# Performance work log

Measured on AMD Instinct MI355X. Metric: run time of the kernel, lower is better.

The kernel has to match this reference:

```python
import jax, jax.numpy as jnp
import numpy as np

B, S, D, H, DFF = 2, 2048, 1024, 16, 4096
DK = D // H
EPS = 1e-05


def setup_inputs() -> dict:
    key = jax.random.key(0)
    ks = jax.random.split(key, 10)
    s = 0.02
    return {
        "x": jax.random.normal(ks[0], (B, S, D), jnp.float32),
        "src_mask": jnp.ones((B, 1, 1, S), jnp.int32),
        "wq": jax.random.normal(ks[1], (D, D), jnp.float32) * s,
        "wk": jax.random.normal(ks[2], (D, D), jnp.float32) * s,
        "wv": jax.random.normal(ks[3], (D, D), jnp.float32) * s,
        "wo": jax.random.normal(ks[4], (D, D), jnp.float32) * s,
        "w1": jax.random.normal(ks[5], (D, DFF), jnp.float32) * s,
        "b1": jnp.zeros((DFF,), jnp.float32),
        "w2": jax.random.normal(ks[6], (DFF, D), jnp.float32) * s,
        "b2": jnp.zeros((D,), jnp.float32),
        "gamma1": jnp.ones((), jnp.float32),
        "beta1": jnp.ones((), jnp.float32),
        "gamma2": jnp.ones((), jnp.float32),
        "beta2": jnp.ones((), jnp.float32),
    }


def layer_norm(x, gamma, beta):
    # torch.var uses unbiased estimator (ddof=1); gamma/beta are scalars
    mean = jnp.mean(x, axis=-1, keepdims=True)
    var = jnp.var(x, axis=-1, keepdims=True, ddof=1)
    return (x - mean) * gamma / jnp.sqrt(var + EPS) + beta


def mha(x, wq, wk, wv, wo):
    # Note: source's masked_fill is non-in-place with discarded result -> mask has no effect.
    q = (x @ wq).reshape(B, S, H, DK).transpose(0, 2, 1, 3)
    k = (x @ wk).reshape(B, S, H, DK).transpose(0, 2, 1, 3)
    v = (x @ wv).reshape(B, S, H, DK).transpose(0, 2, 1, 3)
    scores = jnp.einsum('bhqd,bhkd->bhqk', q, k) / jnp.sqrt(jnp.float32(DK))
    attn = jax.nn.softmax(scores, axis=-1)
    out = jnp.einsum('bhqk,bhkd->bhqd', attn, v)
    out = out.transpose(0, 2, 1, 3).reshape(B, S, D)
    return out @ wo


def reference(x, src_mask, wq, wk, wv, wo, w1, b1, w2, b2,
              gamma1, beta1, gamma2, beta2):
    # residual 1: attention (dropout = identity in eval)
    x = layer_norm(x + mha(x, wq, wk, wv, wo), gamma1, beta1)
    # residual 2: FFN
    ff = jax.nn.relu(x @ w1 + b1) @ w2 + b2
    x = layer_norm(x + ff, gamma2, beta2)
    return x
```

## Files before the change

kernel.cpp:

```cpp
#include <hip/hip_runtime.h>
#include <cstdio>

constexpr int B_   = 2;
constexpr int S_   = 2048;
constexpr int D_   = 1024;
constexpr int H_   = 16;
constexpr int DFF_ = 4096;
constexpr int DK_  = D_ / H_;
constexpr int M_   = B_ * S_;
constexpr float EPS_ = 1e-5f;
constexpr size_t MEGE = 1u << 20;
constexpr size_t QKV_STRIDE = 4 * MEGE;

typedef __attribute__((ext_vector_type(8))) short bf16x8;
typedef __attribute__((ext_vector_type(4))) float f32x4;

__device__ __forceinline__ float bf2f(unsigned int u) {
    return __uint_as_float(u << 16);
}
__device__ __forceinline__ unsigned short f2bf(float f) {
    unsigned int u = __float_as_uint(f);
    unsigned int r = u + 0x7fffu + ((u >> 16) & 1u);
    return (unsigned short)(r >> 16);
}
__device__ __forceinline__ unsigned short f2bf_rz(float f) {
    return (unsigned short)(__float_as_uint(f) >> 16);
}

__device__ __forceinline__ void gload_lds16(const unsigned short* g, unsigned short* l) {
    __builtin_amdgcn_global_load_lds(
        (const __attribute__((address_space(1))) unsigned int*)g,
        (__attribute__((address_space(3))) unsigned int*)l, 16, 0, 0);
}

__global__ __launch_bounds__(256)
void tconv_k(const float* __restrict__ W, unsigned short* __restrict__ Wt, int K, int N)
{
    __shared__ float t[32][33];
    const int tx = threadIdx.x & 31, ty = threadIdx.x >> 5;
    const int n0 = blockIdx.x * 32, k0 = blockIdx.y * 32;
    #pragma unroll
    for (int p = 0; p < 4; ++p)
        t[ty + p * 8][tx] = W[(size_t)(k0 + ty + p * 8) * N + n0 + tx];
    __syncthreads();
    #pragma unroll
    for (int p = 0; p < 4; ++p)
        Wt[(size_t)(n0 + ty + p * 8) * K + k0 + tx] = f2bf(t[tx][ty + p * 8]);
}

__global__ __launch_bounds__(256)
void tconv4_k(const float* __restrict__ a, const float* __restrict__ b,
              const float* __restrict__ c, const float* __restrict__ d,
              unsigned short* __restrict__ oa, unsigned short* __restrict__ ob,
              unsigned short* __restrict__ oc, unsigned short* __restrict__ od)
{
    const int z = blockIdx.z;
    const float* W = (z == 0) ? a : (z == 1) ? b : (z == 2) ? c : d;
    unsigned short* Wt = (z == 0) ? oa : (z == 1) ? ob : (z == 2) ? oc : od;
    __shared__ float t[32][33];
    const int tx = threadIdx.x & 31, ty = threadIdx.x >> 5;
    const int n0 = blockIdx.x * 32, k0 = blockIdx.y * 32;
    #pragma unroll
    for (int p = 0; p < 4; ++p)
        t[ty + p * 8][tx] = W[(size_t)(k0 + ty + p * 8) * D_ + n0 + tx];
    __syncthreads();
    #pragma unroll
    for (int p = 0; p < 4; ++p)
        Wt[(size_t)(n0 + ty + p * 8) * D_ + k0 + tx] = f2bf(t[tx][ty + p * 8]);
}

__global__ __launch_bounds__(256)
void cvtx_k(const float* __restrict__ in, unsigned short* __restrict__ out) {
    int i = blockIdx.x * 256 + threadIdx.x;
    float4 f = reinterpret_cast<const float4*>(in)[i];
    ushort4 u;
    u.x = f2bf(f.x); u.y = f2bf(f.y); u.z = f2bf(f.z); u.w = f2bf(f.w);
    reinterpret_cast<ushort4*>(out)[i] = u;
}

template<int BM, int OMODE, bool RELU>
__global__ __launch_bounds__(512, 2)
void mg2_k(const unsigned short* __restrict__ A,
           const unsigned short* __restrict__ Bt,
           const float* __restrict__ bias,
           unsigned short* __restrict__ C,
           int M, int N, int K, int Kld)
{
    constexpr int MI  = BM / 64;
    constexpr int AMH = (BM == 128) ? 2 : 1;
    __shared__ __align__(16) unsigned short As[2][BM * 64];
    __shared__ __align__(16) unsigned short Bs[2][256 * 64];

    const int z = blockIdx.z;
    A  += (size_t)z * K;
    Bt += (size_t)z * K;
    C  += (size_t)z * ((size_t)M * N);

    const int tid  = threadIdx.x;
    const int w    = tid >> 6, lane = tid & 63;
    const int l15  = lane & 15, quad = lane >> 4;
    const int wm   = w >> 2, wn = w & 3;
    const int m0   = blockIdx.y * BM, n0 = blockIdx.x * 256;
    const int NT   = K >> 6;

    const int srow = lane >> 3;
    const int schk = (lane & 7) ^ srow;
    const int rsw  = l15 & 7;

    f32x4 acc[2][MI][2][2];
    #pragma unroll
    for (int mh = 0; mh < 2; ++mh)
        #pragma unroll
        for (int mi = 0; mi < MI; ++mi)
            #pragma unroll
            for (int nh = 0; nh < 2; ++nh)
                #pragma unroll
                for (int nj = 0; nj < 2; ++nj)
                    acc[mh][mi][nh][nj] = (f32x4){0.f, 0.f, 0.f, 0.f};

    bf16x8 aA[AMH][MI][2];
    bf16x8 b0[2][2], b1[2][2];

    auto stage = [&](int tile, int type) {
        if (tile >= NT) return;
        const int buf = tile & 1;
        unsigned short* dst; const unsigned short* src; int r0;
        if (BM == 256) {
            if      (type == 0) { dst = &As[buf][0];        src = A;  r0 = m0; }
            else if (type == 1) { dst = &Bs[buf][0];        src = Bt; r0 = n0; }
            else if (type == 2) { dst = &Bs[buf][128 * 64]; src = Bt; r0 = n0 + 128; }
            else                { dst = &As[buf][128 * 64]; src = A;  r0 = m0 + 128; }
        } else {
            if      (type == 0) { dst = &Bs[buf][0];        src = Bt; r0 = n0; }
            else if (type == 1) { dst = &As[buf][0];        src = A;  r0 = m0; }
            else                { dst = &Bs[buf][128 * 64]; src = Bt; r0 = n0 + 128; }
        }
        const int k0 = tile * 64;
        #pragma unroll
        for (int g = 0; g < 2; ++g) {
            const int r = w * 16 + g * 8 + srow;
            gload_lds16(src + (size_t)(r0 + r) * Kld + k0 + schk * 8,
                        dst + (w * 16 + g * 8) * 64);
        }
    };
    auto rdA = [&](int buf, int mh, int amh) {
        const unsigned short* base = &As[buf][(BM == 256 && mh) ? 128 * 64 : 0];
        #pragma unroll
        for (int mi = 0; mi < MI; ++mi) {
            const int row = (BM == 256) ? (wm * 64 + mi * 16 + l15)
                                        : (wm * 64 + mh * 32 + mi * 16 + l15);
            const unsigned short* rp = base + row * 64;
            aA[amh][mi][0] = *reinterpret_cast<const bf16x8*>(rp + ((quad    ) ^ rsw) * 8);
            aA[amh][mi][1] = *reinterpret_cast<const bf16x8*>(rp + ((quad + 4) ^ rsw) * 8);
        }
    };
    auto rdB = [&](int buf, int nh, bf16x8 (&b)[2][2]) {
        const unsigned short* base = &Bs[buf][nh ? 128 * 64 : 0];
        #pragma unroll
        for (int nj = 0; nj < 2; ++nj) {
            const int row = wn * 32 + nj * 16 + l15;
            const unsigned short* rp = base + row * 64;
            b[nj][0] = *reinterpret_cast<const bf16x8*>(rp + ((quad    ) ^ rsw) * 8);
            b[nj][1] = *reinterpret_cast<const bf16x8*>(rp + ((quad + 4) ^ rsw) * 8);
        }
    };
    auto mm = [&](int mh, int amh, int nh, bf16x8 (&b)[2][2]) {
        __builtin_amdgcn_s_setprio(1);
        #pragma unroll
        for (int mi = 0; mi < MI; ++mi)
            #pragma unroll
            for (int nj = 0; nj < 2; ++nj) {
                acc[mh][mi][nh][nj] = __builtin_amdgcn_mfma_f32_16x16x32_bf16(
                    aA[amh][mi][0], b[nj][0], acc[mh][mi][nh][nj], 0, 0, 0);
                acc[mh][mi][nh][nj] = __builtin_amdgcn_mfma_f32_16x16x32_bf16(
                    aA[amh][mi][1], b[nj][1], acc[mh][mi][nh][nj], 0, 0, 0);
            }
        __builtin_amdgcn_s_setprio(0);
    };

    if (BM == 256) {
        stage(0, 0); stage(0, 1); stage(0, 2); stage(0, 3);
        stage(1, 0); stage(1, 1); stage(1, 2);
    } else {
        stage(0, 0); stage(0, 1); stage(0, 2);
        stage(1, 0); stage(1, 1);
    }

    for (int t = 0; t < NT; ++t) {
        const int cur = t & 1;
        if (t == NT - 1)    asm volatile("s_waitcnt vmcnt(0)" ::: "memory");
        else if (BM == 256) asm volatile("s_waitcnt vmcnt(6)" ::: "memory");
        else                asm volatile("s_waitcnt vmcnt(4)" ::: "memory");
        __builtin_amdgcn_s_barrier();

        if (BM == 256) {
            rdA(cur, 0, 0); rdB(cur, 0, b0); stage(t + 1, 3);
            __builtin_amdgcn_s_barrier();
            asm volatile("s_waitcnt lgkmcnt(0)" ::: "memory");
            mm(0, 0, 0, b0);
            __builtin_amdgcn_s_barrier();
            rdB(cur, 1, b1); stage(t + 2, 0);
            __builtin_amdgcn_s_barrier();
            asm volatile("s_waitcnt lgkmcnt(0)" ::: "memory");
            mm(0, 0, 1, b1);
            __builtin_amdgcn_s_barrier();
            rdA(cur, 1, 0); stage(t + 2, 1);
            __builtin_amdgcn_s_barrier();
            asm volatile("s_waitcnt lgkmcnt(0)" ::: "memory");
            mm(1, 0, 0, b0);
            __builtin_amdgcn_s_barrier();
            stage(t + 2, 2);
            __builtin_amdgcn_s_barrier();
            asm volatile("s_waitcnt lgkmcnt(0)" ::: "memory");
            mm(1, 0, 1, b1);
        } else {
            rdA(cur, 0, 0); rdA(cur, 1, 1); rdB(cur, 0, b0); stage(t + 1, 2);
            __builtin_amdgcn_s_barrier();
            asm volatile("s_waitcnt lgkmcnt(0)" ::: "memory");
            mm(0, 0, 0, b0); mm(1, 1, 0, b0);
            __builtin_amdgcn_s_barrier();
            rdB(cur, 1, b1); stage(t + 2, 0); stage(t + 2, 1);
            __builtin_amdgcn_s_barrier();
            asm volatile("s_waitcnt lgkmcnt(0)" ::: "memory");
            mm(0, 0, 1, b1); mm(1, 1, 1, b1);
        }
    }

    #pragma unroll
    for (int mh = 0; mh < 2; ++mh)
        #pragma unroll
        for (int mi = 0; mi < MI; ++mi) {
            const int mrow = (BM == 256) ? (mh * 128 + wm * 64 + mi * 16)
                                         : (wm * 64 + mh * 32 + mi * 16);
            #pragma unroll
            for (int r = 0; r < 4; ++r) {
                const int m = m0 + mrow + quad * 4 + r;
                #pragma unroll
                for (int nh = 0; nh < 2; ++nh)
                    #pragma unroll
                    for (int nj = 0; nj < 2; ++nj) {
                        const int n = n0 + nh * 128 + wn * 32 + nj * 16 + l15;
                        float v = acc[mh][mi][nh][nj][r];
                        if (bias) v += bias[n];
                        if (RELU) v = fmaxf(v, 0.0f);
                        size_t o;
                        if (OMODE == 2) {
                            int mat = n >> 10, nn = n & 1023;
                            int b = m >> 11, s = m & 2047;
                            int h = nn >> 6, dk = nn & 63;
                            o = (size_t)mat * QKV_STRIDE + (((size_t)b * H_ + h) * S_ + s) * DK_ + dk;
                        } else {
                            o = (size_t)m * N + n;
                        }
                        C[o] = f2bf(v);
                    }
            }
        }
}

__device__ __forceinline__ float wave_sum(float v) {
    #pragma unroll
    for (int off = 32; off > 0; off >>= 1) v += __shfl_down(v, off, 64);
    return v;
}

constexpr int TQ_ = 128;
constexpr int TK_ = 64;
constexpr int LP_ = 72;
constexpr int NT_ = S_ / TK_;

__global__ __launch_bounds__(256)
void fattn_k(const unsigned short* __restrict__ Qm, const unsigned short* __restrict__ Km,
             const unsigned short* __restrict__ Vm, unsigned short* __restrict__ O)
{
    const int bh  = blockIdx.x >> 4;
    const int qt  = blockIdx.x & 15;
    const int tid = threadIdx.x;
    const int w = tid >> 6, lane = tid & 63;
    const int quad = lane >> 4, l15 = lane & 15;

    __shared__ unsigned short Ks[2][TK_][LP_];
    __shared__ unsigned short Vt[2][DK_ + 16][LP_];
    __shared__ unsigned short Ps[4][32][LP_];

    bf16x8 qf[2][2];
    #pragma unroll
    for (int i = 0; i < 2; ++i) {
        const unsigned short* qp = Qm + ((size_t)bh * S_ + qt * TQ_ + w * 32 + i * 16 + l15) * DK_;
        qf[i][0] = *reinterpret_cast<const bf16x8*>(qp + quad * 8);
        qf[i][1] = *reinterpret_cast<const bf16x8*>(qp + 32 + quad * 8);
    }

    f32x4 o[2][4];
    f32x4 o4[2];
    #pragma unroll
    for (int i = 0; i < 2; ++i) {
        #pragma unroll
        for (int n = 0; n < 4; ++n) o[i][n] = (f32x4){0.f, 0.f, 0.f, 0.f};
        o4[i] = (f32x4){0.f, 0.f, 0.f, 0.f};
    }

    const unsigned short* kg0 = Km + (size_t)bh * S_ * DK_;
    const unsigned short* vg0 = Vm + (size_t)bh * S_ * DK_;
    const int dgrp = tid >> 4;
    const int vkp  = tid & 15;

    {
        const uint4* kg = reinterpret_cast<const uint4*>(kg0);
        #pragma unroll
        for (int p = 0; p < 2; ++p) {
            int idx = p * 256 + tid;
            *reinterpret_cast<uint4*>(&Ks[0][idx >> 3][(idx & 7) * 8]) = kg[idx];
        }
        ushort4 vp[4];
        #pragma unroll
        for (int p = 0; p < 4; ++p)
            vp[p] = reinterpret_cast<const ushort4*>(vg0 + (size_t)(vkp + p * 16) * DK_)[dgrp];
        ushort4 pk;
        pk.x = vp[0].x; pk.y = vp[1].x; pk.z = vp[2].x; pk.w = vp[3].x;
        *reinterpret_cast<ushort4*>(&Vt[0][dgrp * 4 + 0][vkp * 4]) = pk;
        pk.x = vp[0].y; pk.y = vp[1].y; pk.z = vp[2].y; pk.w = vp[3].y;
        *reinterpret_cast<ushort4*>(&Vt[0][dgrp * 4 + 1][vkp * 4]) = pk;
        pk.x = vp[0].z; pk.y = vp[1].z; pk.z = vp[2].z; pk.w = vp[3].z;
        *reinterpret_cast<ushort4*>(&Vt[0][dgrp * 4 + 2][vkp * 4]) = pk;
        pk.x = vp[0].w; pk.y = vp[1].w; pk.z = vp[2].w; pk.w = vp[3].w;
        *reinterpret_cast<ushort4*>(&Vt[0][dgrp * 4 + 3][vkp * 4]) = pk;
        for (int idx = tid; idx < 2 * 16 * LP_; idx += 256) {
            int b  = idx / (16 * LP_);
            int rr = (idx / LP_) % 16;
            int cc = idx % LP_;
            Vt[b][64 + rr][cc] = (rr == 0) ? (unsigned short)0x3F80 : (unsigned short)0;
        }
    }

    for (int t = 0; t < NT_; ++t) {
        const int cur = t & 1, nxt = cur ^ 1;
        __syncthreads();

        uint4 kpre0, kpre1;
        ushort4 vp[4];
        const bool hn = (t + 1 < NT_);
        if (hn) {
            const uint4* kg = reinterpret_cast<const uint4*>(kg0 + (size_t)(t + 1) * TK_ * DK_);
            kpre0 = kg[tid];
            kpre1 = kg[256 + tid];
            const unsigned short* vg = vg0 + (size_t)(t + 1) * TK_ * DK_;
            #pragma unroll
            for (int p = 0; p < 4; ++p)
                vp[p] = reinterpret_cast<const ushort4*>(vg + (size_t)(vkp + p * 16) * DK_)[dgrp];
        }

        f32x4 s[2][4];
        #pragma unroll
        for (int n = 0; n < 4; ++n) {
            bf16x8 b0 = *reinterpret_cast<const bf16x8*>(&Ks[cur][n * 16 + l15][quad * 8]);
            bf16x8 b1 = *reinterpret_cast<const bf16x8*>(&Ks[cur][n * 16 + l15][32 + quad * 8]);
            #pragma unroll
            for (int i = 0; i < 2; ++i) {
                f32x4 a2 = (f32x4){0.f, 0.f, 0.f, 0.f};
                a2 = __builtin_amdgcn_mfma_f32_16x16x32_bf16(qf[i][0], b0, a2, 0, 0, 0);
                a2 = __builtin_amdgcn_mfma_f32_16x16x32_bf16(qf[i][1], b1, a2, 0, 0, 0);
                s[i][n] = a2;
            }
        }

        #pragma unroll
        for (int i = 0; i < 2; ++i)
            #pragma unroll
            for (int r = 0; r < 4; ++r) {
                ushort4 pk;
                pk.x = f2bf_rz(__expf(s[i][0][r] * 0.125f));
                pk.y = f2bf_rz(__expf(s[i][1][r] * 0.125f));
                pk.z = f2bf_rz(__expf(s[i][2][r] * 0.125f));
                pk.w = f2bf_rz(__expf(s[i][3][r] * 0.125f));
                *reinterpret_cast<ushort4*>(&Ps[w][i * 16 + quad * 4 + r][l15 * 4]) = pk;
            }

        if (hn) {
            *reinterpret_cast<uint4*>(&Ks[nxt][tid >> 3][(tid & 7) * 8]) = kpre0;
            int idx = 256 + tid;
            *reinterpret_cast<uint4*>(&Ks[nxt][idx >> 3][(idx & 7) * 8]) = kpre1;
            ushort4 pk;
            pk.x = vp[0].x; pk.y = vp[1].x; pk.z = vp[2].x; pk.w = vp[3].x;
            *reinterpret_cast<ushort4*>(&Vt[nxt][dgrp * 4 + 0][vkp * 4]) = pk;
            pk.x = vp[0].y; pk.y = vp[1].y; pk.z = vp[2].y; pk.w = vp[3].y;
            *reinterpret_cast<ushort4*>(&Vt[nxt][dgrp * 4 + 1][vkp * 4]) = pk;
            pk.x = vp[0].z; pk.y = vp[1].z; pk.z = vp[2].z; pk.w = vp[3].z;
            *reinterpret_cast<ushort4*>(&Vt[nxt][dgrp * 4 + 2][vkp * 4]) = pk;
            pk.x = vp[0].w; pk.y = vp[1].w; pk.z = vp[2].w; pk.w = vp[3].w;
            *reinterpret_cast<ushort4*>(&Vt[nxt][dgrp * 4 + 3][vkp * 4]) = pk;
        }
        __syncthreads();

        bf16x8 pa[2][2];
        #pragma unroll
        for (int i = 0; i < 2; ++i) {
            pa[i][0] = *reinterpret_cast<const bf16x8*>(&Ps[w][i * 16 + l15][quad * 8]);
            pa[i][1] = *reinterpret_cast<const bf16x8*>(&Ps[w][i * 16 + l15][32 + quad * 8]);
        }
        #pragma unroll
        for (int n = 0; n < 4; ++n) {
            bf16x8 vb0 = *reinterpret_cast<const bf16x8*>(&Vt[cur][n * 16 + l15][quad * 8]);
            bf16x8 vb1 = *reinterpret_cast<const bf16x8*>(&Vt[cur][n * 16 + l15][32 + quad * 8]);
            #pragma unroll
            for (int i = 0; i < 2; ++i) {
                o[i][n] = __builtin_amdgcn_mfma_f32_16x16x32_bf16(pa[i][0], vb0, o[i][n], 0, 0, 0);
                o[i][n] = __builtin_amdgcn_mfma_f32_16x16x32_bf16(pa[i][1], vb1, o[i][n], 0, 0, 0);
            }
        }
        {
            bf16x8 vb40 = *reinterpret_cast<const bf16x8*>(&Vt[cur][64 + l15][quad * 8]);
            bf16x8 vb41 = *reinterpret_cast<const bf16x8*>(&Vt[cur][64 + l15][32 + quad * 8]);
            #pragma unroll
            for (int i = 0; i < 2; ++i) {
                o4[i] = __builtin_amdgcn_mfma_f32_16x16x32_bf16(pa[i][0], vb40, o4[i], 0, 0, 0);
                o4[i] = __builtin_amdgcn_mfma_f32_16x16x32_bf16(pa[i][1], vb41, o4[i], 0, 0, 0);
            }
        }
    }

    const int b = bh >> 4, h = bh & 15;
    #pragma unroll
    for (int i = 0; i < 2; ++i)
        #pragma unroll
        for (int r = 0; r < 4; ++r) {
            float lrv = __shfl(o4[i][r], lane & 0x30, 64);
            float inv = 1.0f / lrv;
            int q = qt * TQ_ + w * 32 + i * 16 + quad * 4 + r;
            unsigned short* op = O + ((size_t)b * S_ + q) * D_ + h * DK_;
            #pragma unroll
            for (int n = 0; n < 4; ++n)
                op[n * 16 + l15] = f2bf(o[i][n][r] * inv);
        }
}

template<bool HAS_BIAS, bool RES_F32, bool OUT_F32>
__global__ __launch_bounds__(256)
void lnr_k(const unsigned short* __restrict__ P0, const unsigned short* __restrict__ P1,
           const void* __restrict__ res, const float* __restrict__ bias,
           const float* __restrict__ gp, const float* __restrict__ bp,
           void* __restrict__ Out)
{
    const int row = blockIdx.x;
    const int tid = threadIdx.x;
    const int lane = tid & 63, wave = tid >> 6;
    __shared__ float rs[4], rss[4];

    const size_t i4 = (size_t)row * 256 + tid;
    const ushort4 a = reinterpret_cast<const ushort4*>(P0)[i4];
    const ushort4 b = reinterpret_cast<const ushort4*>(P1)[i4];
    float v0 = bf2f(a.x) + bf2f(b.x);
    float v1 = bf2f(a.y) + bf2f(b.y);
    float v2 = bf2f(a.z) + bf2f(b.z);
    float v3 = bf2f(a.w) + bf2f(b.w);
    if (RES_F32) {
        float4 rv = reinterpret_cast<const float4*>(res)[i4];
        v0 += rv.x; v1 += rv.y; v2 += rv.z; v3 += rv.w;
    } else {
        ushort4 rv = reinterpret_cast<const ushort4*>(res)[i4];
        v0 += bf2f(rv.x); v1 += bf2f(rv.y); v2 += bf2f(rv.z); v3 += bf2f(rv.w);
    }
    if (HAS_BIAS) {
        float4 bv = reinterpret_cast<const float4*>(bias)[tid];
        v0 += bv.x; v1 += bv.y; v2 += bv.z; v3 += bv.w;
    }

    float s  = v0 + v1 + v2 + v3;
    float ss = v0*v0 + v1*v1 + v2*v2 + v3*v3;
    s = wave_sum(s);
    ss = wave_sum(ss);
    if (lane == 0) { rs[wave] = s; rss[wave] = ss; }
    __syncthreads();
    const float stot  = rs[0] + rs[1] + rs[2] + rs[3];
    const float sstot = rss[0] + rss[1] + rss[2] + rss[3];
    const float mean = stot / (float)D_;
    const float var  = (sstot - (float)D_ * mean * mean) / (float)(D_ - 1);
    const float scl = gp[0] * rsqrtf(var + EPS_);
    const float be = bp[0];

    float o0 = (v0 - mean) * scl + be;
    float o1 = (v1 - mean) * scl + be;
    float o2 = (v2 - mean) * scl + be;
    float o3 = (v3 - mean) * scl + be;
    if (OUT_F32) {
        reinterpret_cast<float4*>(Out)[i4] = make_float4(o0, o1, o2, o3);
    } else {
        ushort4 o;
        o.x = f2bf(o0); o.y = f2bf(o1); o.z = f2bf(o2); o.w = f2bf(o3);
        reinterpret_cast<ushort4*>(Out)[i4] = o;
    }
}

extern "C" void kernel_launch(void* const* d_in, const int* in_sizes, int n_in,
                              void* d_out, int out_size, void* d_ws, size_t ws_size,
                              hipStream_t stream)
{
    const float* x   = (const float*)d_in[0];
    const float* wq  = (const float*)d_in[2];
    const float* wk  = (const float*)d_in[3];
    const float* wv  = (const float*)d_in[4];
    const float* wo  = (const float*)d_in[5];
    const float* w1  = (const float*)d_in[6];
    const float* b1  = (const float*)d_in[7];
    const float* w2  = (const float*)d_in[8];
    const float* b2  = (const float*)d_in[9];
    const float* g1  = (const float*)d_in[10];
    const float* be1 = (const float*)d_in[11];
    const float* g2  = (const float*)d_in[12];
    const float* be2 = (const float*)d_in[13];

    unsigned short* ws = (unsigned short*)d_ws;
    const size_t need_bytes = 32 * MEGE * 2;
    if (ws_size < need_bytes) {
        fprintf(stderr, "kernel_launch: ws too small (%zu < %zu)\n", ws_size, need_bytes);
    }
    unsigned short* wqt = ws + 0 * MEGE;
    unsigned short* wkt = ws + 1 * MEGE;
    unsigned short* wvt = ws + 2 * MEGE;
    unsigned short* wot = ws + 3 * MEGE;
    unsigned short* w1t = ws + 4 * MEGE;
    unsigned short* w2t = ws + 8 * MEGE;
    unsigned short* xb  = ws + 12 * MEGE;
    unsigned short* Q   = ws + 16 * MEGE;
    unsigned short* K   = ws + 20 * MEGE;
    unsigned short* V   = ws + 24 * MEGE;
    unsigned short* AO  = ws + 28 * MEGE;
    unsigned short* x1  = xb;
    unsigned short* WP  = ws + 16 * MEGE;
    unsigned short* h1  = ws + 16 * MEGE;
    unsigned short* FP  = ws + 0 * MEGE;

    tconv4_k<<<dim3(D_ / 32, D_ / 32, 4), 256, 0, stream>>>(wq, wk, wv, wo, wqt, wkt, wvt, wot);
    tconv_k<<<dim3(DFF_ / 32, D_ / 32), 256, 0, stream>>>(w1, w1t, D_, DFF_);
    tconv_k<<<dim3(D_ / 32, DFF_ / 32), 256, 0, stream>>>(w2, w2t, DFF_, D_);
    cvtx_k<<<dim3(M_ * D_ / 1024), 256, 0, stream>>>(x, xb);

    mg2_k<256, 2, false><<<dim3(3 * D_ / 256, M_ / 256), 512, 0, stream>>>(
        xb, wqt, nullptr, Q, M_, 3 * D_, D_, D_);

    fattn_k<<<dim3(B_ * H_ * (S_ / TQ_)), 256, 0, stream>>>(Q, K, V, AO);

    mg2_k<128, 0, false><<<dim3(D_ / 256, M_ / 128, 2), 512, 0, stream>>>(
        AO, wot, nullptr, WP, M_, D_, D_ / 2, D_);

    lnr_k<false, true, false><<<dim3(M_), 256, 0, stream>>>(
        WP, WP + 4 * MEGE, x, nullptr, g1, be1, x1);

    mg2_k<256, 0, true><<<dim3(DFF_ / 256, M_ / 256), 512, 0, stream>>>(
        x1, w1t, b1, h1, M_, DFF_, D_, D_);

    mg2_k<128, 0, false><<<dim3(D_ / 256, M_ / 128, 2), 512, 0, stream>>>(
        h1, w2t, nullptr, FP, M_, D_, DFF_ / 2, DFF_);

    lnr_k<true, false, true><<<dim3(M_), 256, 0, stream>>>(
        FP, FP + 4 * MEGE, x1, b2, g2, be2, d_out);
}
```

Measured before the change: 347.4 us.

## Swizzle attention LDS tiles, async K staging, drop a barrier, fuse prep kernels

Replaces the padded LDS tiles in the flash-attention kernel with XOR-swizzled 64-wide layouts. K tiles are now staged with direct global-to-LDS loads, and the mid-iteration barrier between P writes and P/V reads is removed. MFMA sections get raised wave priority. The four weight/input conversion kernels are merged into one launch. The intent is to cut LDS bank conflicts, register staging and launch overhead; the removed barrier risks ordering hazards, since Vt[nxt] and Ks[nxt] writes still rely on the top-of-loop barrier.

After: 342.3 us. Within noise of the previous version (-1.5%).

```diff
diff --git a/kernel.cpp b/kernel.cpp
--- a/kernel.cpp
+++ b/kernel.cpp
@@ -33,49 +33,50 @@
         (__attribute__((address_space(3))) unsigned int*)l, 16, 0, 0);
 }
 
+__device__ __forceinline__ void tr32(const float* __restrict__ W, unsigned short* __restrict__ Wt,
+                                     int K, int N, int bx, int by, float* t )
+{
+    const int tx = threadIdx.x & 31, ty = threadIdx.x >> 5;
+    const int n0 = bx * 32, k0 = by * 32;
+    #pragma unroll
+    for (int p = 0; p < 4; ++p)
+        t[(ty + p * 8) * 33 + tx] = W[(size_t)(k0 + ty + p * 8) * N + n0 + tx];
+    __syncthreads();
+    #pragma unroll
+    for (int p = 0; p < 4; ++p)
+        Wt[(size_t)(n0 + ty + p * 8) * K + k0 + tx] = f2bf(t[tx * 33 + ty + p * 8]);
+}
+
 __global__ __launch_bounds__(256)
-void tconv_k(const float* __restrict__ W, unsigned short* __restrict__ Wt, int K, int N)
+void prep_k(const float* __restrict__ wq, const float* __restrict__ wk,
+            const float* __restrict__ wv, const float* __restrict__ wo,
+            const float* __restrict__ w1, const float* __restrict__ w2,
+            const float* __restrict__ x,
+            unsigned short* __restrict__ wqt, unsigned short* __restrict__ wkt,
+            unsigned short* __restrict__ wvt, unsigned short* __restrict__ wot,
+            unsigned short* __restrict__ w1t, unsigned short* __restrict__ w2t,
+            unsigned short* __restrict__ xb)
 {
-    __shared__ float t[32][33];
-    const int tx = threadIdx.x & 31, ty = threadIdx.x >> 5;
-    const int n0 = blockIdx.x * 32, k0 = blockIdx.y * 32;
-    #pragma unroll
-    for (int p = 0; p < 4; ++p)
-        t[ty + p * 8][tx] = W[(size_t)(k0 + ty + p * 8) * N + n0 + tx];
-    __syncthreads();
-    #pragma unroll
-    for (int p = 0; p < 4; ++p)
-        Wt[(size_t)(n0 + ty + p * 8) * K + k0 + tx] = f2bf(t[tx][ty + p * 8]);
-}
-
-__global__ __launch_bounds__(256)
-void tconv4_k(const float* __restrict__ a, const float* __restrict__ b,
-              const float* __restrict__ c, const float* __restrict__ d,
-              unsigned short* __restrict__ oa, unsigned short* __restrict__ ob,
-              unsigned short* __restrict__ oc, unsigned short* __restrict__ od)
-{
-    const int z = blockIdx.z;
-    const float* W = (z == 0) ? a : (z == 1) ? b : (z == 2) ? c : d;
-    unsigned short* Wt = (z == 0) ? oa : (z == 1) ? ob : (z == 2) ? oc : od;
-    __shared__ float t[32][33];
-    const int tx = threadIdx.x & 31, ty = threadIdx.x >> 5;
-    const int n0 = blockIdx.x * 32, k0 = blockIdx.y * 32;
-    #pragma unroll
-    for (int p = 0; p < 4; ++p)
-        t[ty + p * 8][tx] = W[(size_t)(k0 + ty + p * 8) * D_ + n0 + tx];
-    __syncthreads();
-    #pragma unroll
-    for (int p = 0; p < 4; ++p)
-        Wt[(size_t)(n0 + ty + p * 8) * D_ + k0 + tx] = f2bf(t[tx][ty + p * 8]);
-}
-
-__global__ __launch_bounds__(256)
-void cvtx_k(const float* __restrict__ in, unsigned short* __restrict__ out) {
-    int i = blockIdx.x * 256 + threadIdx.x;
-    float4 f = reinterpret_cast<const float4*>(in)[i];
-    ushort4 u;
-    u.x = f2bf(f.x); u.y = f2bf(f.y); u.z = f2bf(f.z); u.w = f2bf(f.w);
-    reinterpret_cast<ushort4*>(out)[i] = u;
+    __shared__ float t[32 * 33];
+    const int bid = blockIdx.x;
+    if (bid < 4096) {
+        const int z = bid >> 10, rem = bid & 1023;
+        const float* W = (z == 0) ? wq : (z == 1) ? wk : (z == 2) ? wv : wo;
+        unsigned short* Wt = (z == 0) ? wqt : (z == 1) ? wkt : (z == 2) ? wvt : wot;
+        tr32(W, Wt, D_, D_, rem & 31, rem >> 5, t);
+    } else if (bid < 8192) {
+        const int rem = bid - 4096;
+        tr32(w1, w1t, D_, DFF_, rem & 127, rem >> 7, t);
+    } else if (bid < 12288) {
+        const int rem = bid - 8192;
+        tr32(w2, w2t, DFF_, D_, rem & 31, rem >> 5, t);
+    } else {
+        const int i = (bid - 12288) * 256 + threadIdx.x;
+        float4 f = reinterpret_cast<const float4*>(x)[i];
+        ushort4 u;
+        u.x = f2bf(f.x); u.y = f2bf(f.y); u.z = f2bf(f.z); u.w = f2bf(f.w);
+        reinterpret_cast<ushort4*>(xb)[i] = u;
+    }
 }
 
 template<int BM, int OMODE, bool RELU>
@@ -266,7 +267,6 @@
 
 constexpr int TQ_ = 128;
 constexpr int TK_ = 64;
-constexpr int LP_ = 72;
 constexpr int NT_ = S_ / TK_;
 
 __global__ __launch_bounds__(256)
@@ -278,10 +278,11 @@
     const int tid = threadIdx.x;
     const int w = tid >> 6, lane = tid & 63;
     const int quad = lane >> 4, l15 = lane & 15;
-
-    __shared__ unsigned short Ks[2][TK_][LP_];
-    __shared__ unsigned short Vt[2][DK_ + 16][LP_];
-    __shared__ unsigned short Ps[4][32][LP_];
+    const int sw = l15 & 7;
+
+    __shared__ __align__(16) unsigned short Ks[2][TK_][64];
+    __shared__ __align__(16) unsigned short Vt[2][80][64];
+    __shared__ __align__(16) unsigned short Ps[4][32][64];
 
     bf16x8 qf[2][2];
     #pragma unroll
@@ -304,32 +305,48 @@
     const unsigned short* vg0 = Vm + (size_t)bh * S_ * DK_;
     const int dgrp = tid >> 4;
     const int vkp  = tid & 15;
-
-    {
-        const uint4* kg = reinterpret_cast<const uint4*>(kg0);
-        #pragma unroll
-        for (int p = 0; p < 2; ++p) {
-            int idx = p * 256 + tid;
-            *reinterpret_cast<uint4*>(&Ks[0][idx >> 3][(idx & 7) * 8]) = kg[idx];
-        }
-        ushort4 vp[4];
+    const int srow = lane >> 3;
+    const int schk = (lane & 7) ^ srow;
+
+    auto stageK = [&](int t, int buf) {
+        const unsigned short* src = kg0 + (size_t)t * TK_ * DK_;
+        #pragma unroll
+        for (int g = 0; g < 2; ++g) {
+            const int r0 = w * 16 + g * 8;
+            gload_lds16(src + (size_t)(r0 + srow) * DK_ + schk * 8, &Ks[buf][r0][0]);
+        }
+    };
+    auto loadV = [&](int t, ushort4 (&vp)[4]) {
+        const unsigned short* vg = vg0 + (size_t)t * TK_ * DK_;
         #pragma unroll
         for (int p = 0; p < 4; ++p)
-            vp[p] = reinterpret_cast<const ushort4*>(vg0 + (size_t)(vkp + p * 16) * DK_)[dgrp];
+            vp[p] = reinterpret_cast<const ushort4*>(vg + (size_t)(vkp + p * 16) * DK_)[dgrp];
+    };
+    auto storeVt = [&](int buf, ushort4 (&vp)[4]) {
+        char* base = reinterpret_cast<char*>(&Vt[buf][dgrp * 4][0]);
+        const int cs = vkp >> 1, ch = (vkp & 1) << 3;
         ushort4 pk;
         pk.x = vp[0].x; pk.y = vp[1].x; pk.z = vp[2].x; pk.w = vp[3].x;
-        *reinterpret_cast<ushort4*>(&Vt[0][dgrp * 4 + 0][vkp * 4]) = pk;
+        *reinterpret_cast<ushort4*>(base + 0 * 128 + (((cs ^ ((dgrp * 4 + 0) & 7)) << 4) + ch)) = pk;
         pk.x = vp[0].y; pk.y = vp[1].y; pk.z = vp[2].y; pk.w = vp[3].y;
-        *reinterpret_cast<ushort4*>(&Vt[0][dgrp * 4 + 1][vkp * 4]) = pk;
+        *reinterpret_cast<ushort4*>(base + 1 * 128 + (((cs ^ ((dgrp * 4 + 1) & 7)) << 4) + ch)) = pk;
         pk.x = vp[0].z; pk.y = vp[1].z; pk.z = vp[2].z; pk.w = vp[3].z;
-        *reinterpret_cast<ushort4*>(&Vt[0][dgrp * 4 + 2][vkp * 4]) = pk;
+        *reinterpret_cast<ushort4*>(base + 2 * 128 + (((cs ^ ((dgrp * 4 + 2) & 7)) << 4) + ch)) = pk;
         pk.x = vp[0].w; pk.y = vp[1].w; pk.z = vp[2].w; pk.w = vp[3].w;
-        *reinterpret_cast<ushort4*>(&Vt[0][dgrp * 4 + 3][vkp * 4]) = pk;
-        for (int idx = tid; idx < 2 * 16 * LP_; idx += 256) {
-            int b  = idx / (16 * LP_);
-            int rr = (idx / LP_) % 16;
-            int cc = idx % LP_;
-            Vt[b][64 + rr][cc] = (rr == 0) ? (unsigned short)0x3F80 : (unsigned short)0;
+        *reinterpret_cast<ushort4*>(base + 3 * 128 + (((cs ^ ((dgrp * 4 + 3) & 7)) << 4) + ch)) = pk;
+    };
+
+    stageK(0, 0);
+    {
+        ushort4 vp0[4];
+        loadV(0, vp0);
+        storeVt(0, vp0);
+        for (int idx = tid; idx < 2 * 16 * 64; idx += 256) {
+            const int b  = idx >> 10;
+            const int rr = (idx >> 6) & 15;
+            const int cc = idx & 63;
+            Vt[b][64 + rr][((cc >> 3) ^ (rr & 7)) * 8 + (cc & 7)] =
+                (rr == 0) ? (unsigned short)0x3F80 : (unsigned short)0;
         }
     }
 
@@ -337,24 +354,17 @@
         const int cur = t & 1, nxt = cur ^ 1;
         __syncthreads();
 
-        uint4 kpre0, kpre1;
+        const bool hn = (t + 1 < NT_);
         ushort4 vp[4];
-        const bool hn = (t + 1 < NT_);
-        if (hn) {
-            const uint4* kg = reinterpret_cast<const uint4*>(kg0 + (size_t)(t + 1) * TK_ * DK_);
-            kpre0 = kg[tid];
-            kpre1 = kg[256 + tid];
-            const unsigned short* vg = vg0 + (size_t)(t + 1) * TK_ * DK_;
-            #pragma unroll
-            for (int p = 0; p < 4; ++p)
-                vp[p] = reinterpret_cast<const ushort4*>(vg + (size_t)(vkp + p * 16) * DK_)[dgrp];
-        }
+        if (hn) { stageK(t + 1, nxt); loadV(t + 1, vp); }
 
         f32x4 s[2][4];
+        __builtin_amdgcn_s_setprio(1);
         #pragma unroll
         for (int n = 0; n < 4; ++n) {
-            bf16x8 b0 = *reinterpret_cast<const bf16x8*>(&Ks[cur][n * 16 + l15][quad * 8]);
-            bf16x8 b1 = *reinterpret_cast<const bf16x8*>(&Ks[cur][n * 16 + l15][32 + quad * 8]);
+            const unsigned short* kp = &Ks[cur][n * 16 + l15][0];
+            bf16x8 b0 = *reinterpret_cast<const bf16x8*>(kp + ((quad ^ sw) << 3));
+            bf16x8 b1 = *reinterpret_cast<const bf16x8*>(kp + (((quad + 4) ^ sw) << 3));
             #pragma unroll
             for (int i = 0; i < 2; ++i) {
                 f32x4 a2 = (f32x4){0.f, 0.f, 0.f, 0.f};
@@ -363,6 +373,7 @@
                 s[i][n] = a2;
             }
         }
+        __builtin_amdgcn_s_setprio(0);
 
         #pragma unroll
         for (int i = 0; i < 2; ++i)
@@ -373,35 +384,27 @@
                 pk.y = f2bf_rz(__expf(s[i][1][r] * 0.125f));
                 pk.z = f2bf_rz(__expf(s[i][2][r] * 0.125f));
                 pk.w = f2bf_rz(__expf(s[i][3][r] * 0.125f));
-                *reinterpret_cast<ushort4*>(&Ps[w][i * 16 + quad * 4 + r][l15 * 4]) = pk;
+                const int R = i * 16 + quad * 4 + r;
+                *reinterpret_cast<ushort4*>(
+                    reinterpret_cast<char*>(&Ps[w][R][0]) +
+                    ((((l15 >> 1) ^ (R & 7)) << 4) + ((l15 & 1) << 3))) = pk;
             }
 
-        if (hn) {
-            *reinterpret_cast<uint4*>(&Ks[nxt][tid >> 3][(tid & 7) * 8]) = kpre0;
-            int idx = 256 + tid;
-            *reinterpret_cast<uint4*>(&Ks[nxt][idx >> 3][(idx & 7) * 8]) = kpre1;
-            ushort4 pk;
-            pk.x = vp[0].x; pk.y = vp[1].x; pk.z = vp[2].x; pk.w = vp[3].x;
-            *reinterpret_cast<ushort4*>(&Vt[nxt][dgrp * 4 + 0][vkp * 4]) = pk;
-            pk.x = vp[0].y; pk.y = vp[1].y; pk.z = vp[2].y; pk.w = vp[3].y;
-            *reinterpret_cast<ushort4*>(&Vt[nxt][dgrp * 4 + 1][vkp * 4]) = pk;
-            pk.x = vp[0].z; pk.y = vp[1].z; pk.z = vp[2].z; pk.w = vp[3].z;
-            *reinterpret_cast<ushort4*>(&Vt[nxt][dgrp * 4 + 2][vkp * 4]) = pk;
-            pk.x = vp[0].w; pk.y = vp[1].w; pk.z = vp[2].w; pk.w = vp[3].w;
-            *reinterpret_cast<ushort4*>(&Vt[nxt][dgrp * 4 + 3][vkp * 4]) = pk;
-        }
-        __syncthreads();
+        if (hn) storeVt(nxt, vp);
 
         bf16x8 pa[2][2];
         #pragma unroll
         for (int i = 0; i < 2; ++i) {
-            pa[i][0] = *reinterpret_cast<const bf16x8*>(&Ps[w][i * 16 + l15][quad * 8]);
-            pa[i][1] = *reinterpret_cast<const bf16x8*>(&Ps[w][i * 16 + l15][32 + quad * 8]);
-        }
+            const unsigned short* pp = &Ps[w][i * 16 + l15][0];
+            pa[i][0] = *reinterpret_cast<const bf16x8*>(pp + ((quad ^ sw) << 3));
+            pa[i][1] = *reinterpret_cast<const bf16x8*>(pp + (((quad + 4) ^ sw) << 3));
+        }
+        __builtin_amdgcn_s_setprio(1);
         #pragma unroll
         for (int n = 0; n < 4; ++n) {
-            bf16x8 vb0 = *reinterpret_cast<const bf16x8*>(&Vt[cur][n * 16 + l15][quad * 8]);
-            bf16x8 vb1 = *reinterpret_cast<const bf16x8*>(&Vt[cur][n * 16 + l15][32 + quad * 8]);
+            const unsigned short* vb = &Vt[cur][n * 16 + l15][0];
+            bf16x8 vb0 = *reinterpret_cast<const bf16x8*>(vb + ((quad ^ sw) << 3));
+            bf16x8 vb1 = *reinterpret_cast<const bf16x8*>(vb + (((quad + 4) ^ sw) << 3));
             #pragma unroll
             for (int i = 0; i < 2; ++i) {
                 o[i][n] = __builtin_amdgcn_mfma_f32_16x16x32_bf16(pa[i][0], vb0, o[i][n], 0, 0, 0);
@@ -409,14 +412,16 @@
             }
         }
         {
-            bf16x8 vb40 = *reinterpret_cast<const bf16x8*>(&Vt[cur][64 + l15][quad * 8]);
-            bf16x8 vb41 = *reinterpret_cast<const bf16x8*>(&Vt[cur][64 + l15][32 + quad * 8]);
+            const unsigned short* vb = &Vt[cur][64 + l15][0];
+            bf16x8 vb40 = *reinterpret_cast<const bf16x8*>(vb + ((quad ^ sw) << 3));
+            bf16x8 vb41 = *reinterpret_cast<const bf16x8*>(vb + (((quad + 4) ^ sw) << 3));
             #pragma unroll
             for (int i = 0; i < 2; ++i) {
                 o4[i] = __builtin_amdgcn_mfma_f32_16x16x32_bf16(pa[i][0], vb40, o4[i], 0, 0, 0);
                 o4[i] = __builtin_amdgcn_mfma_f32_16x16x32_bf16(pa[i][1], vb41, o4[i], 0, 0, 0);
             }
         }
+        __builtin_amdgcn_s_setprio(0);
     }
 
     const int b = bh >> 4, h = bh & 15;
@@ -530,10 +535,8 @@
     unsigned short* h1  = ws + 16 * MEGE;
     unsigned short* FP  = ws + 0 * MEGE;
 
-    tconv4_k<<<dim3(D_ / 32, D_ / 32, 4), 256, 0, stream>>>(wq, wk, wv, wo, wqt, wkt, wvt, wot);
-    tconv_k<<<dim3(DFF_ / 32, D_ / 32), 256, 0, stream>>>(w1, w1t, D_, DFF_);
-    tconv_k<<<dim3(D_ / 32, DFF_ / 32), 256, 0, stream>>>(w2, w2t, DFF_, D_);
-    cvtx_k<<<dim3(M_ * D_ / 1024), 256, 0, stream>>>(x, xb);
+    prep_k<<<dim3(16384), 256, 0, stream>>>(wq, wk, wv, wo, w1, w2, x,
+                                            wqt, wkt, wvt, wot, w1t, w2t, xb);
 
     mg2_k<256, 2, false><<<dim3(3 * D_ / 256, M_ / 256), 512, 0, stream>>>(
         xb, wqt, nullptr, Q, M_, 3 * D_, D_, D_);
```
